# Performance work log

Measured on AMD Instinct MI355X. Metric: run time of the kernel, lower is better.

Reference implementation:

```python
import jax, jax.numpy as jnp
import numpy as np

N = 4096
E = 262144
IN_C = 128
OUT_C = 128
EDGE_D = 16


def setup_inputs() -> dict:
    key = jax.random.key(0)
    k = jax.random.split(key, 8)
    x = jax.random.normal(k[0], (N, IN_C), dtype=jnp.float32)
    edge_index = jax.random.randint(k[1], (2, E), 0, N, dtype=jnp.int64)
    edge_attr = jax.random.normal(k[2], (N, N, EDGE_D), dtype=jnp.float32)
    # nn.Linear params: y = x @ W.T + b; store pre-transposed W for x @ W
    s1 = 1.0 / np.sqrt(IN_C + EDGE_D)
    s2 = 1.0 / np.sqrt(OUT_C)
    W1 = jax.random.uniform(k[3], (IN_C + EDGE_D, OUT_C), jnp.float32, -s1, s1)
    b1 = jax.random.uniform(k[4], (OUT_C,), jnp.float32, -s1, s1)
    W2 = jax.random.uniform(k[5], (OUT_C, OUT_C), jnp.float32, -s2, s2)
    b2 = jax.random.uniform(k[6], (OUT_C,), jnp.float32, -s2, s2)
    return {"x": x, "edge_index": edge_index, "edge_attr": edge_attr,
            "W1": W1, "b1": b1, "W2": W2, "b2": b2}


def reference(x, edge_index, edge_attr, W1, b1, W2, b2):
    row, col = edge_index[0], edge_index[1]
    x_row = x[row]                      # [E, IN_C] gather
    e = edge_attr[row, col]             # [E, EDGE_D] gather from dense NxN table
    h = jnp.concatenate([x_row, e], axis=-1)     # [E, IN_C+EDGE_D]
    h = jax.nn.relu(h @ W1 + b1)                  # [E, OUT_C]
    h = jax.nn.relu(h @ W2 + b2)                  # [E, OUT_C]
    # global_add_pool(out, col): scatter-add edges into node buckets by col
    return jax.ops.segment_sum(h, col, num_segments=x.shape[0])  # [N, OUT_C]
```

## Files before the change

kernel.cpp:

```cpp
#include <hip/hip_runtime.h>
#include <hip/hip_bf16.h>

#define NN 4096
#define IC 128
#define OC 128
#define ED 16
#define EPB 128
#define NT 512
#define NSLOT 8
#define NBLK 256

typedef __bf16 bf16x8 __attribute__((ext_vector_type(8)));
typedef float  f32x16 __attribute__((ext_vector_type(16)));

#define BAR() do { asm volatile("s_waitcnt lgkmcnt(0)" ::: "memory"); \
    __builtin_amdgcn_s_barrier(); \
    __builtin_amdgcn_sched_barrier(0); } while (0)

__device__ __forceinline__ unsigned short bf16u(float f) {
    unsigned int u = __float_as_uint(f);
    u = (u + 0x7FFFu + ((u >> 16) & 1u)) >> 16;
    return (unsigned short)u;
}
__device__ __forceinline__ float bf16tof(unsigned short h) {
    return __uint_as_float(((unsigned int)h) << 16);
}
__device__ __forceinline__ int swzk(int row) { return (row ^ (row >> 3)) & 7; }

__global__ __launch_bounds__(128) void k_xw1(
    const float* __restrict__ x, const float* __restrict__ W1,
    const float* __restrict__ b1, float* __restrict__ xw1b,
    float* __restrict__ out, int* __restrict__ hist)
{
    __shared__ float xs[8][IC];
    const int t = threadIdx.x;
    const int r0 = blockIdx.x * 8;
    #pragma unroll
    for (int r = 0; r < 8; ++r) xs[r][t] = x[(size_t)(r0 + r) * IC + t];

    const float4 z = make_float4(0.f, 0.f, 0.f, 0.f);
    float4* o4 = (float4*)out;
    o4[blockIdx.x * 256 + t]       = z;
    o4[blockIdx.x * 256 + 128 + t] = z;
    if (blockIdx.x == 0) {
        int4* h4 = (int4*)hist;
        #pragma unroll
        for (int j = 0; j < 8; ++j) h4[j * 128 + t] = make_int4(0, 0, 0, 0);
    }

    __syncthreads();
    float acc[8];
    const float bb = b1[t];
    #pragma unroll
    for (int r = 0; r < 8; ++r) acc[r] = bb;
    #pragma unroll 4
    for (int k = 0; k < IC; ++k) {
        const float w = W1[(size_t)k * OC + t];
        #pragma unroll
        for (int r = 0; r < 8; ++r) acc[r] = fmaf(xs[r][k], w, acc[r]);
    }
    #pragma unroll
    for (int r = 0; r < 8; ++r) xw1b[(size_t)(r0 + r) * OC + t] = acc[r];
}

__global__ void k_hist(const int* __restrict__ eidx, int* __restrict__ hist, int E) {
    const int i = blockIdx.x * blockDim.x + threadIdx.x;
    if (i < E) atomicAdd(&hist[eidx[E + i]], 1);
}

__global__ __launch_bounds__(256) void k_scan(
    const int* __restrict__ hist, int* __restrict__ cursor)
{
    __shared__ int tot[256];
    __shared__ int base[256];
    const int t = threadIdx.x;
    int loc[16];
    int s = 0;
    #pragma unroll
    for (int j = 0; j < 16; ++j) { loc[j] = s; s += hist[t * 16 + j]; }
    tot[t] = s;
    __syncthreads();
    if (t == 0) {
        int a = 0;
        for (int i = 0; i < 256; ++i) { base[i] = a; a += tot[i]; }
    }
    __syncthreads();
    const int b = base[t];
    #pragma unroll
    for (int j = 0; j < 16; ++j) cursor[t * 16 + j] = b + loc[j];
}

__global__ void k_scatter(const int* __restrict__ eidx, int* __restrict__ cursor,
                          int2* __restrict__ csr, int E) {
    const int i = blockIdx.x * blockDim.x + threadIdx.x;
    if (i < E) {
        const int row = eidx[i];
        const int col = eidx[E + i];
        const int pos = atomicAdd(&cursor[col], 1);
        csr[pos] = make_int2(row, col);
    }
}

__global__ __launch_bounds__(NT, 2) void k_edge7(
    const int2* __restrict__ csr, const float* __restrict__ eattr,
    const float* __restrict__ xw1b, const float* __restrict__ W1,
    const float* __restrict__ W2, const float* __restrict__ b2,
    float* __restrict__ out, int E)
{
    extern __shared__ char smem[];
    char*   const h1hi = smem;
    char*   const h1lo = smem + 32768;
    float4* const eaL  = (float4*)(smem + 65536);
    float4* const w1L  = (float4*)(smem + 73728);
    float*  const lacc = (float*)(smem + 81920);
    int*    const srowL = (int*)(smem + 86016);
    int*    const scolL = srowL + 256;

    const int t   = threadIdx.x;
    const int l   = t & 63;
    const int wid = t >> 6;
    const int cg  = t & 15, eg = t >> 4;
    const int c0  = cg << 3, e0 = eg << 2;
    const int sz  = (eg >> 1) & 3;
    const int em  = t >> 2, q = t & 3;
    const int esz = (em >> 3) & 3;

    const int ntl = wid & 3;
    const int mh  = wid >> 2;
    const int lm  = l & 31;
    const int hi  = l >> 5;
    const int c2  = ntl * 32 + lm;

    w1L[t] = ((const float4*)(W1 + (size_t)IC * OC))[t];

    bf16x8 w2h[8], w2l[8];
    #pragma unroll
    for (int s = 0; s < 8; ++s) {
        union { unsigned short us[8]; bf16x8 v; } Uh, Ul;
        #pragma unroll
        for (int j = 0; j < 8; ++j) {
            const float w = W2[(size_t)(s * 16 + hi * 8 + j) * OC + c2];
            const unsigned short h = bf16u(w);
            Uh.us[j] = h;
            Ul.us[j] = bf16u(w - bf16tof(h));
        }
        w2h[s] = Uh.v; w2l[s] = Ul.v;
    }
    const float b2s = b2[c2];

    lacc[t] = 0.f; lacc[t + NT] = 0.f;

    const int nper = (E / EPB) / NBLK;
    const int ibb  = blockIdx.x * nper;

    if (t < EPB) {
        const int2 rc = csr[(size_t)ibb * EPB + t];
        srowL[t] = rc.x;
        scolL[t] = rc.y;
    }
    __syncthreads();

    float4 pA;
    {
        const int r = srowL[em], c = scolL[em];
        pA = ((const float4*)(eattr + ((size_t)r * NN + c) * ED))[q];
    }
    int2 pidx;
    {
        const int ibn = (nper > 1) ? 1 : 0;
        pidx = (t < EPB) ? csr[(size_t)(ibb + ibn) * EPB + t] : make_int2(0, 0);
    }

    int cur = 0;
    for (int ii = 0; ii < nper; ++ii) {
        const int nxt = cur ^ 1;

        BAR();

        if (t < EPB) { srowL[nxt * 128 + t] = pidx.x; scolL[nxt * 128 + t] = pidx.y; }
        eaL[(em * 4 + q) ^ esz] = pA;
        float4 xa[4], xb[4];
        #pragma unroll
        for (int ri = 0; ri < 4; ++ri) {
            const int row = srowL[cur * 128 + e0 + ri];
            const float4* p = (const float4*)(xw1b + (size_t)row * OC + c0);
            xa[ri] = p[0]; xb[ri] = p[1];
        }
        BAR();

        float4 ha[4], hb[4];
        #pragma unroll
        for (int ri = 0; ri < 4; ++ri) { ha[ri] = xa[ri]; hb[ri] = xb[ri]; }
        #pragma unroll
        for (int dc = 0; dc < 4; ++dc) {
            float4 ev[4];
            #pragma unroll
            for (int ri = 0; ri < 4; ++ri)
                ev[ri] = eaL[((e0 + ri) * 4 + dc) ^ sz];
            #pragma unroll
            for (int dd = 0; dd < 4; ++dd) {
                const int d = dc * 4 + dd;
                const float4 wA = w1L[d * 32 + cg * 2];
                const float4 wB = w1L[d * 32 + cg * 2 + 1];
                #pragma unroll
                for (int ri = 0; ri < 4; ++ri) {
                    const float evd = (dd == 0) ? ev[ri].x : (dd == 1) ? ev[ri].y
                                     : (dd == 2) ? ev[ri].z : ev[ri].w;
                    ha[ri].x = fmaf(evd, wA.x, ha[ri].x);
                    ha[ri].y = fmaf(evd, wA.y, ha[ri].y);
                    ha[ri].z = fmaf(evd, wA.z, ha[ri].z);
                    ha[ri].w = fmaf(evd, wA.w, ha[ri].w);
                    hb[ri].x = fmaf(evd, wB.x, hb[ri].x);
                    hb[ri].y = fmaf(evd, wB.y, hb[ri].y);
                    hb[ri].z = fmaf(evd, wB.z, hb[ri].z);
                    hb[ri].w = fmaf(evd, wB.w, hb[ri].w);
                }
            }
        }
        #pragma unroll
        for (int ri = 0; ri < 4; ++ri) {
            const int row = e0 + ri;
            float v[8] = { ha[ri].x, ha[ri].y, ha[ri].z, ha[ri].w,
                           hb[ri].x, hb[ri].y, hb[ri].z, hb[ri].w };
            union { unsigned short us[8]; uint4 qv; } Hh, Hl;
            #pragma unroll
            for (int j = 0; j < 8; ++j) {
                const float f = fmaxf(v[j], 0.f);
                const unsigned short h = bf16u(f);
                Hh.us[j] = h;
                Hl.us[j] = bf16u(f - bf16tof(h));
            }
            const int boff = (cg * 16) ^ (swzk(row) << 4);
            *(uint4*)(h1hi + row * 256 + boff) = Hh.qv;
            *(uint4*)(h1lo + row * 256 + boff) = Hl.qv;
        }
        {
            const int r = srowL[nxt * 128 + em], c = scolL[nxt * 128 + em];
            pA = ((const float4*)(eattr + ((size_t)r * NN + c) * ED))[q];
        }
        {
            const int iin = (ii + 2 < nper) ? (ii + 2) : (nper - 1);
            pidx = (t < EPB) ? csr[(size_t)(ibb + iin) * EPB + t] : make_int2(0, 0);
        }
        BAR();

        f32x16 acc0 = (f32x16)(0.0f);
        f32x16 acc1 = (f32x16)(0.0f);
        const int arow0 = (mh * 2 + 0) * 32 + lm;
        const int arow1 = (mh * 2 + 1) * 32 + lm;
        const int ak0 = swzk(arow0) << 4;
        const int ak1 = swzk(arow1) << 4;
        #pragma unroll
        for (int s = 0; s < 8; ++s) {
            const int kb = s * 32 + hi * 16;
            const bf16x8 aH0 = *(const bf16x8*)(h1hi + arow0 * 256 + (kb ^ ak0));
            const bf16x8 aL0 = *(const bf16x8*)(h1lo + arow0 * 256 + (kb ^ ak0));
            const bf16x8 aH1 = *(const bf16x8*)(h1hi + arow1 * 256 + (kb ^ ak1));
            const bf16x8 aL1 = *(const bf16x8*)(h1lo + arow1 * 256 + (kb ^ ak1));
            acc0 = __builtin_amdgcn_mfma_f32_32x32x16_bf16(aH0, w2h[s], acc0, 0, 0, 0);
            acc1 = __builtin_amdgcn_mfma_f32_32x32x16_bf16(aH1, w2h[s], acc1, 0, 0, 0);
            acc0 = __builtin_amdgcn_mfma_f32_32x32x16_bf16(aL0, w2h[s], acc0, 0, 0, 0);
            acc1 = __builtin_amdgcn_mfma_f32_32x32x16_bf16(aL1, w2h[s], acc1, 0, 0, 0);
            acc0 = __builtin_amdgcn_mfma_f32_32x32x16_bf16(aH0, w2l[s], acc0, 0, 0, 0);
            acc1 = __builtin_amdgcn_mfma_f32_32x32x16_bf16(aH1, w2l[s], acc1, 0, 0, 0);
        }

        const int colbase = scolL[cur * 128];
        #pragma unroll
        for (int p = 0; p < 2; ++p) {
            const int mbase = (mh * 2 + p) * 32 + 4 * hi;
            #pragma unroll
            for (int g = 0; g < 4; ++g) {
                const int eb = mbase + 8 * g;
                float sv;
                {
                    const float a0 = (p == 0) ? acc0[4 * g] : acc1[4 * g];
                    sv = fmaxf(a0 + b2s, 0.f);
                }
                int ccur = scolL[cur * 128 + eb];
                #pragma unroll
                for (int j = 1; j < 4; ++j) {
                    const float aj = (p == 0) ? acc0[4 * g + j] : acc1[4 * g + j];
                    const float v = fmaxf(aj + b2s, 0.f);
                    const int c = scolL[cur * 128 + eb + j];
                    if (c == ccur) {
                        sv += v;
                    } else {
                        const int slot = ccur - colbase;
                        if (slot < NSLOT) {
                            if (sv != 0.f) atomicAdd(&lacc[slot * OC + c2], sv);
                        } else {
                            if (sv != 0.f) atomicAdd(&out[(size_t)ccur * OC + c2], sv);
                        }
                        ccur = c; sv = v;
                    }
                }
                const int slot = ccur - colbase;
                if (slot < NSLOT) {
                    if (sv != 0.f) atomicAdd(&lacc[slot * OC + c2], sv);
                } else {
                    if (sv != 0.f) atomicAdd(&out[(size_t)ccur * OC + c2], sv);
                }
            }
        }
        BAR();

        int span = scolL[cur * 128 + 127] - colbase + 1;
        if (span > NSLOT) span = NSLOT;
        for (int idx = t; idx < span * OC; idx += NT) {
            const float v = lacc[idx];
            lacc[idx] = 0.f;
            if (v != 0.f)
                atomicAdd(&out[(size_t)(colbase + (idx >> 7)) * OC + (idx & 127)], v);
        }
        cur = nxt;
    }
}

#define LDS_BYTES 88064

extern "C" void kernel_launch(void* const* d_in, const int* in_sizes, int n_in,
                              void* d_out, int out_size, void* d_ws, size_t ws_size,
                              hipStream_t stream) {
    const float* x    = (const float*)d_in[0];
    const int*   eidx = (const int*)d_in[1];
    const float* ea   = (const float*)d_in[2];
    const float* W1   = (const float*)d_in[3];
    const float* b1   = (const float*)d_in[4];
    const float* W2   = (const float*)d_in[5];
    const float* b2   = (const float*)d_in[6];
    float* out = (float*)d_out;

    const int E = in_sizes[1] / 2;

    char* ws = (char*)d_ws;
    float* xw1b   = (float*)ws;
    int*   hist   = (int*)(ws + 2097152);
    int*   cursor = (int*)(ws + 2097152 + 16384);
    int2*  csr    = (int2*)(ws + 2097152 + 32768);

    k_xw1<<<NN / 8, 128, 0, stream>>>(x, W1, b1, xw1b, out, hist);
    k_hist<<<(E + 255) / 256, 256, 0, stream>>>(eidx, hist, E);
    k_scan<<<1, 256, 0, stream>>>(hist, cursor);
    k_scatter<<<(E + 255) / 256, 256, 0, stream>>>(eidx, cursor, csr, E);

    hipFuncSetAttribute(reinterpret_cast<const void*>(k_edge7),
                        hipFuncAttributeMaxDynamicSharedMemorySize, LDS_BYTES);
    k_edge7<<<NBLK, NT, LDS_BYTES, stream>>>(csr, ea, xw1b, W1, W2, b2, out, E);
}
```

Measured before the change: 150.4 us.

## Fuse preprocessing and edge kernels into one persistent kernel with grid barriers

```diff
diff --git a/kernel.cpp b/kernel.cpp
--- a/kernel.cpp
+++ b/kernel.cpp
@@ -9,6 +9,7 @@
 #define NT 512
 #define NSLOT 8
 #define NBLK 256
+#define NCPY 8
 
 typedef __bf16 bf16x8 __attribute__((ext_vector_type(8)));
 typedef float  f32x16 __attribute__((ext_vector_type(16)));
@@ -27,87 +28,130 @@
 }
 __device__ __forceinline__ int swzk(int row) { return (row ^ (row >> 3)) & 7; }
 
-__global__ __launch_bounds__(128) void k_xw1(
-    const float* __restrict__ x, const float* __restrict__ W1,
-    const float* __restrict__ b1, float* __restrict__ xw1b,
-    float* __restrict__ out, int* __restrict__ hist)
+__device__ __forceinline__ void gsync(int* cnt, int* gen) {
+    __syncthreads();
+    if (threadIdx.x == 0) {
+        __threadfence();
+        const int my = __hip_atomic_load(gen, __ATOMIC_SEQ_CST,
+                                         __HIP_MEMORY_SCOPE_AGENT);
+        const int arrived = __hip_atomic_fetch_add(cnt, 1, __ATOMIC_SEQ_CST,
+                                                   __HIP_MEMORY_SCOPE_AGENT);
+        if (arrived == NBLK - 1) {
+            __hip_atomic_store(cnt, 0, __ATOMIC_SEQ_CST,
+                               __HIP_MEMORY_SCOPE_AGENT);
+            __hip_atomic_fetch_add(gen, 1, __ATOMIC_SEQ_CST,
+                                   __HIP_MEMORY_SCOPE_AGENT);
+        } else {
+            while (__hip_atomic_load(gen, __ATOMIC_SEQ_CST,
+                                     __HIP_MEMORY_SCOPE_AGENT) == my) {
+                __builtin_amdgcn_s_sleep(8);
+            }
+        }
+        __threadfence();
+    }
+    __syncthreads();
+}
+
+__global__ __launch_bounds__(NT, 2) void k_all(
+    const float* __restrict__ x, const int* __restrict__ eidx,
+    const float* __restrict__ eattr, const float* __restrict__ W1,
+    const float* __restrict__ b1, const float* __restrict__ W2,
+    const float* __restrict__ b2, float* __restrict__ out,
+    float* __restrict__ xw1b, int* __restrict__ hist8,
+    int* __restrict__ cursor8, int* __restrict__ blocksum,
+    int* __restrict__ gbar, int2* __restrict__ csr, int E)
 {
-    __shared__ float xs[8][IC];
-    const int t = threadIdx.x;
-    const int r0 = blockIdx.x * 8;
-    #pragma unroll
-    for (int r = 0; r < 8; ++r) xs[r][t] = x[(size_t)(r0 + r) * IC + t];
-
-    const float4 z = make_float4(0.f, 0.f, 0.f, 0.f);
-    float4* o4 = (float4*)out;
-    o4[blockIdx.x * 256 + t]       = z;
-    o4[blockIdx.x * 256 + 128 + t] = z;
-    if (blockIdx.x == 0) {
-        int4* h4 = (int4*)hist;
-        #pragma unroll
-        for (int j = 0; j < 8; ++j) h4[j * 128 + t] = make_int4(0, 0, 0, 0);
-    }
-
-    __syncthreads();
-    float acc[8];
-    const float bb = b1[t];
-    #pragma unroll
-    for (int r = 0; r < 8; ++r) acc[r] = bb;
-    #pragma unroll 4
-    for (int k = 0; k < IC; ++k) {
-        const float w = W1[(size_t)k * OC + t];
-        #pragma unroll
-        for (int r = 0; r < 8; ++r) acc[r] = fmaf(xs[r][k], w, acc[r]);
-    }
-    #pragma unroll
-    for (int r = 0; r < 8; ++r) xw1b[(size_t)(r0 + r) * OC + t] = acc[r];
-}
-
-__global__ void k_hist(const int* __restrict__ eidx, int* __restrict__ hist, int E) {
-    const int i = blockIdx.x * blockDim.x + threadIdx.x;
-    if (i < E) atomicAdd(&hist[eidx[E + i]], 1);
-}
-
-__global__ __launch_bounds__(256) void k_scan(
-    const int* __restrict__ hist, int* __restrict__ cursor)
-{
-    __shared__ int tot[256];
-    __shared__ int base[256];
-    const int t = threadIdx.x;
-    int loc[16];
-    int s = 0;
-    #pragma unroll
-    for (int j = 0; j < 16; ++j) { loc[j] = s; s += hist[t * 16 + j]; }
-    tot[t] = s;
+    extern __shared__ char smem[];
+    const int t   = threadIdx.x;
+    const int bid = blockIdx.x;
+
+    ((float4*)out)[bid * NT + t] = make_float4(0.f, 0.f, 0.f, 0.f);
+
+    {
+        const int row = bid * 16 + (t >> 5);
+        const int c4  = (t & 31) * 4;
+        float4 a = make_float4(b1[c4], b1[c4 + 1], b1[c4 + 2], b1[c4 + 3]);
+        const float4* xr = (const float4*)(x + (size_t)row * IC);
+        #pragma unroll 8
+        for (int k4 = 0; k4 < 32; ++k4) {
+            const float4 xv = xr[k4];
+            const float4 w0 = *(const float4*)(W1 + (size_t)(k4 * 4 + 0) * OC + c4);
+            const float4 w1v = *(const float4*)(W1 + (size_t)(k4 * 4 + 1) * OC + c4);
+            const float4 w2v = *(const float4*)(W1 + (size_t)(k4 * 4 + 2) * OC + c4);
+            const float4 w3v = *(const float4*)(W1 + (size_t)(k4 * 4 + 3) * OC + c4);
+            a.x = fmaf(xv.x, w0.x, a.x); a.y = fmaf(xv.x, w0.y, a.y);
+            a.z = fmaf(xv.x, w0.z, a.z); a.w = fmaf(xv.x, w0.w, a.w);
+            a.x = fmaf(xv.y, w1v.x, a.x); a.y = fmaf(xv.y, w1v.y, a.y);
+            a.z = fmaf(xv.y, w1v.z, a.z); a.w = fmaf(xv.y, w1v.w, a.w);
+            a.x = fmaf(xv.z, w2v.x, a.x); a.y = fmaf(xv.z, w2v.y, a.y);
+            a.z = fmaf(xv.z, w2v.z, a.z); a.w = fmaf(xv.z, w2v.w, a.w);
+            a.x = fmaf(xv.w, w3v.x, a.x); a.y = fmaf(xv.w, w3v.y, a.y);
+            a.z = fmaf(xv.w, w3v.z, a.z); a.w = fmaf(xv.w, w3v.w, a.w);
+        }
+        *(float4*)(xw1b + (size_t)row * OC + c4) = a;
+    }
+
+    {
+        const int k  = bid & (NCPY - 1);
+        const int e0 = bid * 1024;
+        #pragma unroll
+        for (int j = 0; j < 2; ++j)
+            atomicAdd(&hist8[k * 4096 + eidx[E + e0 + t + j * NT]], 1);
+    }
+    gsync(gbar, gbar + 1);
+
+    int* sbl = (int*)smem;
+    int* loc = sbl + 16;
+    int* bsl = sbl + 32;
+    if (t < 16) {
+        const int bin = bid * 16 + t;
+        int sb = 0;
+        #pragma unroll
+        for (int k = 0; k < NCPY; ++k) sb += hist8[k * 4096 + bin];
+        sbl[t] = sb;
+    }
     __syncthreads();
     if (t == 0) {
         int a = 0;
-        for (int i = 0; i < 256; ++i) { base[i] = a; a += tot[i]; }
-    }
-    __syncthreads();
-    const int b = base[t];
-    #pragma unroll
-    for (int j = 0; j < 16; ++j) cursor[t * 16 + j] = b + loc[j];
-}
-
-__global__ void k_scatter(const int* __restrict__ eidx, int* __restrict__ cursor,
-                          int2* __restrict__ csr, int E) {
-    const int i = blockIdx.x * blockDim.x + threadIdx.x;
-    if (i < E) {
-        const int row = eidx[i];
-        const int col = eidx[E + i];
-        const int pos = atomicAdd(&cursor[col], 1);
-        csr[pos] = make_int2(row, col);
-    }
-}
-
-__global__ __launch_bounds__(NT, 2) void k_edge7(
-    const int2* __restrict__ csr, const float* __restrict__ eattr,
-    const float* __restrict__ xw1b, const float* __restrict__ W1,
-    const float* __restrict__ W2, const float* __restrict__ b2,
-    float* __restrict__ out, int E)
-{
-    extern __shared__ char smem[];
+        #pragma unroll
+        for (int j = 0; j < 16; ++j) { loc[j] = a; a += sbl[j]; }
+        blocksum[bid] = a;
+    }
+    gsync(gbar, gbar + 1);
+
+    if (t < 256) bsl[t] = blocksum[t];
+    __syncthreads();
+    if (t == 0) {
+        int a = 0;
+        for (int j = 0; j < bid; ++j) a += bsl[j];
+        sbl[0] = a;
+    }
+    __syncthreads();
+    if (t < 16) {
+        const int bin = bid * 16 + t;
+        int off = sbl[0] + loc[t];
+        #pragma unroll
+        for (int k = 0; k < NCPY; ++k) {
+            cursor8[k * 4096 + bin] = off;
+            off += hist8[k * 4096 + bin];
+        }
+    }
+    gsync(gbar, gbar + 1);
+
+    {
+        const int k  = bid & (NCPY - 1);
+        const int e0 = bid * 1024;
+        #pragma unroll
+        for (int j = 0; j < 2; ++j) {
+            const int e   = e0 + t + j * NT;
+            const int row = eidx[e];
+            const int col = eidx[E + e];
+            const int pos = atomicAdd(&cursor8[k * 4096 + col], 1);
+            csr[pos] = make_int2(row, col);
+        }
+    }
+    gsync(gbar, gbar + 1);
+
     char*   const h1hi = smem;
     char*   const h1lo = smem + 32768;
     float4* const eaL  = (float4*)(smem + 65536);
@@ -116,7 +160,6 @@
     int*    const srowL = (int*)(smem + 86016);
     int*    const scolL = srowL + 256;
 
-    const int t   = threadIdx.x;
     const int l   = t & 63;
     const int wid = t >> 6;
     const int cg  = t & 15, eg = t >> 4;
@@ -151,7 +194,7 @@
     lacc[t] = 0.f; lacc[t + NT] = 0.f;
 
     const int nper = (E / EPB) / NBLK;
-    const int ibb  = blockIdx.x * nper;
+    const int ibb  = bid * nper;
 
     if (t < EPB) {
         const int2 rc = csr[(size_t)ibb * EPB + t];
@@ -334,17 +377,18 @@
     const int E = in_sizes[1] / 2;
 
     char* ws = (char*)d_ws;
-    float* xw1b   = (float*)ws;
-    int*   hist   = (int*)(ws + 2097152);
-    int*   cursor = (int*)(ws + 2097152 + 16384);
-    int2*  csr    = (int2*)(ws + 2097152 + 32768);
-
-    k_xw1<<<NN / 8, 128, 0, stream>>>(x, W1, b1, xw1b, out, hist);
-    k_hist<<<(E + 255) / 256, 256, 0, stream>>>(eidx, hist, E);
-    k_scan<<<1, 256, 0, stream>>>(hist, cursor);
-    k_scatter<<<(E + 255) / 256, 256, 0, stream>>>(eidx, cursor, csr, E);
-
-    hipFuncSetAttribute(reinterpret_cast<const void*>(k_edge7),
+    float* xw1b     = (float*)ws;
+    int*   hist8    = (int*)(ws + 2097152);
+    int*   cursor8  = (int*)(ws + 2228224);
+    int*   blocksum = (int*)(ws + 2359296);
+    int*   gbar     = (int*)(ws + 2360320);
+    int2*  csr      = (int2*)(ws + 2621440);
+
+    hipMemsetAsync(ws + 2097152, 0, 263232, stream);
+
+    hipFuncSetAttribute(reinterpret_cast<const void*>(k_all),
                         hipFuncAttributeMaxDynamicSharedMemorySize, LDS_BYTES);
-    k_edge7<<<NBLK, NT, LDS_BYTES, stream>>>(csr, ea, xw1b, W1, W2, b2, out, E);
-}
+    k_all<<<NBLK, NT, LDS_BYTES, stream>>>(x, eidx, ea, W1, b1, W2, b2,
+                                           out, xw1b, hist8, cursor8,
+                                           blocksum, gbar, csr, E);
+}
```

Result: slower. 279.9 us (+86.1%).
